# Kernel tuning notes

Measured on AMD Instinct MI355X. Metric: run time of the kernel, lower is better.

## Reference

```python
import jax, jax.numpy as jnp
import numpy as np

C = 128      # out_channels
G = 4        # RecConvLayer num_groups
BS, CIN, H, W = 4, 3, 96, 96
GN = 8
EPS = 1e-5


def _conv2d(x, w, b, pad):
    out = jax.lax.conv_general_dilated(
        x, w, (1, 1), [(pad, pad), (pad, pad)],
        dimension_numbers=("NCHW", "OIHW", "NCHW"))
    return out + b[None, :, None, None]


def _prelu(x, a):
    return jnp.maximum(x, 0) + a[0] * jnp.minimum(x, 0)


def _group_norm(x, w, b):
    bs, c, h, wd = x.shape
    xg = x.reshape(bs, GN, c // GN, h, wd)
    mu = xg.mean(axis=(2, 3, 4), keepdims=True)
    var = xg.var(axis=(2, 3, 4), keepdims=True)  # biased, as torch GroupNorm
    xn = ((xg - mu) * jax.lax.rsqrt(var + EPS)).reshape(bs, c, h, wd)
    return xn * w[None, :, None, None] + b[None, :, None, None]


def _single_conv(x, w, b, a, gw, gb, pad):
    # SingleConvLayer in eval mode: Conv2d -> PReLU -> GroupNorm (no noise)
    return _group_norm(_prelu(_conv2d(x, w, b, pad), a), gw, gb)


def _bidir_gru_layer(x, wih, whh, bih, bhh):
    # x: (T,B,Din); wih: (2,3C,Din); whh: (2,3C,C); bih/bhh: (2,3C)
    Cc = whh.shape[-1]
    h0 = jnp.zeros((x.shape[1], Cc), x.dtype)

    def run_dir(gx, wh, bh):
        def step(h, g):
            gh = h @ wh.T + bh
            r = jax.nn.sigmoid(g[:, :Cc] + gh[:, :Cc])
            z = jax.nn.sigmoid(g[:, Cc:2 * Cc] + gh[:, Cc:2 * Cc])
            n = jnp.tanh(g[:, 2 * Cc:] + r * gh[:, 2 * Cc:])
            hn = (1.0 - z) * n + z * h
            return hn, hn
        return jax.lax.scan(step, h0, gx)[1]

    yf = run_dir(x @ wih[0].T + bih[0], whh[0], bhh[0])
    yb = run_dir(x[::-1] @ wih[1].T + bih[1], whh[1], bhh[1])[::-1]
    return jnp.concatenate([yf, yb], axis=-1)  # (T,B,2C)


def _gru2(x, wih0, whh0, bih0, bhh0, wih1, whh1, bih1, bhh1):
    y = _bidir_gru_layer(x, wih0, whh0, bih0, bhh0)
    return _bidir_gru_layer(y, wih1, whh1, bih1, bhh1)


_gru_groups = jax.vmap(_gru2, in_axes=(1, 0, 0, 0, 0, 0, 0, 0, 0), out_axes=1)


def _run_gru(x_tgbc, p):
    out = _gru_groups(x_tgbc, *p)               # (T,G,B,2C)
    t, g, b, _ = out.shape
    return out.reshape(t, g, b, 2, -1).mean(axis=3)  # mean over directions -> (T,G,B,C)


def _forward(x, conv1_w, conv1_b, prelu1_a, gn1_w, gn1_b,
             conv2_w, conv2_b, prelu2_a, gn2_w, gn2_b,
             comb_w, comb_b, prelu3_a, gn3_w, gn3_b,
             h_wih0, h_whh0, h_bih0, h_bhh0, h_wih1, h_whh1, h_bih1, h_bhh1,
             v_wih0, v_whh0, v_bih0, v_bhh0, v_wih1, v_whh1, v_bih1, v_bhh1,
             h1_wih0, h1_whh0, h1_bih0, h1_bhh0, h1_wih1, h1_whh1, h1_bih1, h1_bhh1,
             v1_wih0, v1_whh0, v1_bih0, v1_bhh0, v1_wih1, v1_whh1, v1_bih1, v1_bhh1):
    x = _single_conv(x, conv1_w, conv1_b, prelu1_a, gn1_w, gn1_b, 1)
    x = _single_conv(x, conv2_w, conv2_b, prelu2_a, gn2_w, gn2_b, 1)
    bs, c, m, n = x.shape
    vg, hg = n // G, m // G
    y = jnp.transpose(x, (0, 3, 2, 1))                               # (bs,n,m,c)
    y1 = jnp.transpose(y.reshape(bs, G, vg * m, c), (2, 1, 0, 3))    # vertical seqs (m*vg,G,bs,c)
    ym = jnp.transpose(y, (0, 2, 1, 3))                              # (bs,m,n,c)
    y2 = jnp.transpose(ym.reshape(bs, G, hg * n, c), (2, 1, 0, 3))   # horizontal seqs (n*hg,G,bs,c)

    hn = _run_gru(y2, (h_wih0, h_whh0, h_bih0, h_bhh0, h_wih1, h_whh1, h_bih1, h_bhh1))
    vn = _run_gru(y1, (v_wih0, v_whh0, v_bih0, v_bhh0, v_wih1, v_whh1, v_bih1, v_bhh1))

    hn_b = jnp.transpose(hn, (2, 1, 0, 3)).reshape(bs, m, n, c)
    y1b = jnp.transpose(jnp.transpose(hn_b, (0, 2, 1, 3)).reshape(bs, G, vg * m, c), (2, 1, 0, 3))
    vn_b = jnp.transpose(vn, (2, 1, 0, 3)).reshape(bs, n, m, c)
    y2b = jnp.transpose(jnp.transpose(vn_b, (0, 2, 1, 3)).reshape(bs, G, hg * n, c), (2, 1, 0, 3))

    hn2 = _run_gru(y2b, (h1_wih0, h1_whh0, h1_bih0, h1_bhh0, h1_wih1, h1_whh1, h1_bih1, h1_bhh1))
    vn2 = _run_gru(y1b, (v1_wih0, v1_whh0, v1_bih0, v1_bhh0, v1_wih1, v1_whh1, v1_bih1, v1_bhh1))

    hcnm = jnp.transpose(jnp.transpose(hn2, (2, 1, 0, 3)).reshape(bs, m, n, c), (0, 3, 1, 2))  # (bs,c,m,n)
    vcnm = jnp.transpose(jnp.transpose(vn2, (2, 1, 0, 3)).reshape(bs, n, m, c), (0, 3, 2, 1))  # (bs,c,m,n)
    return _single_conv(jnp.concatenate([hcnm, vcnm], axis=1), comb_w, comb_b, prelu3_a, gn3_w, gn3_b, 0)


def setup_inputs() -> dict:
    key = jax.random.key(0)
    ks = jax.random.split(key, 8)
    nrm = lambda k, s, sc: jax.random.normal(k, s, jnp.float32) * sc
    inp = {
        "x": nrm(ks[0], (BS, CIN, H, W), 1.0),
        "conv1_w": nrm(ks[1], (C, CIN, 3, 3), 0.1), "conv1_b": nrm(ks[2], (C,), 0.05),
        "prelu1_a": jnp.full((1,), 0.25, jnp.float32),
        "gn1_w": jnp.ones((C,), jnp.float32), "gn1_b": jnp.zeros((C,), jnp.float32),
        "conv2_w": nrm(ks[3], (C, C, 3, 3), 0.03), "conv2_b": nrm(ks[4], (C,), 0.05),
        "prelu2_a": jnp.full((1,), 0.25, jnp.float32),
        "gn2_w": jnp.ones((C,), jnp.float32), "gn2_b": jnp.zeros((C,), jnp.float32),
        "comb_w": nrm(ks[5], (C, 2 * C, 1, 1), 0.05), "comb_b": nrm(ks[6], (C,), 0.05),
        "prelu3_a": jnp.full((1,), 0.25, jnp.float32),
        "gn3_w": jnp.ones((C,), jnp.float32), "gn3_b": jnp.zeros((C,), jnp.float32),
    }
    shapes = [("wih0", (G, 2, 3 * C, C)), ("whh0", (G, 2, 3 * C, C)),
              ("bih0", (G, 2, 3 * C)), ("bhh0", (G, 2, 3 * C)),
              ("wih1", (G, 2, 3 * C, 2 * C)), ("whh1", (G, 2, 3 * C, C)),
              ("bih1", (G, 2, 3 * C)), ("bhh1", (G, 2, 3 * C))]
    for i, p in enumerate(["h", "v", "h1", "v1"]):
        kp = jax.random.split(jax.random.fold_in(key, 100 + i), 8)
        for j, (nm, sh) in enumerate(shapes):
            inp[p + "_" + nm] = nrm(kp[j], sh, 0.05)
    return inp


def reference(x, conv1_w, conv1_b, prelu1_a, gn1_w, gn1_b,
              conv2_w, conv2_b, prelu2_a, gn2_w, gn2_b,
              comb_w, comb_b, prelu3_a, gn3_w, gn3_b,
              h_wih0, h_whh0, h_bih0, h_bhh0, h_wih1, h_whh1, h_bih1, h_bhh1,
              v_wih0, v_whh0, v_bih0, v_bhh0, v_wih1, v_whh1, v_bih1, v_bhh1,
              h1_wih0, h1_whh0, h1_bih0, h1_bhh0, h1_wih1, h1_whh1, h1_bih1, h1_bhh1,
              v1_wih0, v1_whh0, v1_bih0, v1_bhh0, v1_wih1, v1_whh1, v1_bih1, v1_bhh1):
    return _forward(x, conv1_w, conv1_b, prelu1_a, gn1_w, gn1_b,
                    conv2_w, conv2_b, prelu2_a, gn2_w, gn2_b,
                    comb_w, comb_b, prelu3_a, gn3_w, gn3_b,
                    h_wih0, h_whh0, h_bih0, h_bhh0, h_wih1, h_whh1, h_bih1, h_bhh1,
                    v_wih0, v_whh0, v_bih0, v_bhh0, v_wih1, v_whh1, v_bih1, v_bhh1,
                    h1_wih0, h1_whh0, h1_bih0, h1_bhh0, h1_wih1, h1_whh1, h1_bih1, h1_bhh1,
                    v1_wih0, v1_whh0, v1_bih0, v1_bhh0, v1_wih1, v1_whh1, v1_bih1, v1_bhh1)
```

## Files before the change

kernel.cpp:

```cpp
#include <hip/hip_runtime.h>

typedef unsigned short u16;
typedef __attribute__((ext_vector_type(8))) short bf16x8;
typedef __attribute__((ext_vector_type(4))) float f32x4;
typedef __attribute__((ext_vector_type(4))) int   i32x4;

#define DEVFN static __device__ __forceinline__
#define AS_G __attribute__((address_space(1)))
#define AS_L __attribute__((address_space(3)))

DEVFN float b2f(u16 u){ return __uint_as_float(((unsigned int)u)<<16); }
DEVFN u16 f2b(float f){ unsigned int x = __float_as_uint(f); x += 0x7FFFu + ((x>>16)&1u); return (u16)(x>>16); }
DEVFN float fastrcp(float x){ return __builtin_amdgcn_rcpf(x); }

struct CastArgs { const float* s[8]; u16* d[8]; int n[8]; };
__global__ void castf2b_g(CastArgs a)
{
    int p = blockIdx.y;
    int i = blockIdx.x*256 + threadIdx.x;
    if (i < a.n[p]) a.d[p][i] = f2b(a.s[p][i]);
}

struct QuantArgs { const float* w[8]; char* q[8]; float* dq[8]; };
__global__ void quant_whh_g(QuantArgs a)
{
    int p = blockIdx.y;
    int row = blockIdx.x;
    int lane = threadIdx.x;
    const float* wr = a.w[p] + (long long)row*128;
    float v0 = wr[lane], v1 = wr[lane+64];
    float m = fmaxf(fabsf(v0), fabsf(v1));
#pragma unroll
    for (int off = 32; off; off >>= 1) m = fmaxf(m, __shfl_xor(m, off));
    float s = (m > 0.f) ? m * (1.f/127.f) : 1.f;
    float inv = 1.f / s;
    a.q[p][(long long)row*128 + lane]      = (char)__float2int_rn(v0 * inv);
    a.q[p][(long long)row*128 + lane + 64] = (char)__float2int_rn(v1 * inv);
    if (lane == 0) a.dq[p][row] = s * (1.f/127.f);
}

__global__ __launch_bounds__(256)
void gemm_bt(const u16* __restrict__ A, const u16* __restrict__ B,
             const float* __restrict__ bias, u16* __restrict__ C,
             int K, int N,
             long long zA, long long zB, long long zBias, long long zC,
             const float* __restrict__ alphaP, float* __restrict__ stats, int rowsPerB,
             const u16* __restrict__ Ax, const u16* __restrict__ Bx,
             const float* __restrict__ biasx, u16* __restrict__ Cx, int zHalf)
{
    __shared__ __align__(16) u16 As[128*32];
    __shared__ __align__(16) u16 Bs[128*32];
    __shared__ float sstat[16];

    const int tid  = threadIdx.x;
    const int wave = tid >> 6, lane = tid & 63;
    const int quad = lane >> 4, l16 = lane & 15;
    const int wm = wave & 1, wn = wave >> 1;

    long long z = blockIdx.z;
    const u16* Ap = A; const u16* Bp = B; const float* bp = bias; u16* Cp = C;
    if (Ax && z >= zHalf) { Ap = Ax; Bp = Bx; bp = biasx; Cp = Cx; z -= zHalf; }
    Ap += z * zA; Bp += z * zB; Cp += z * zC;
    if (bp) bp += z * zBias;

    const int lin   = blockIdx.y * gridDim.x + blockIdx.x;
    const int mBase = (int)(lin / gridDim.y) * 128;
    const int nBase = (int)(lin % gridDim.y) * 128;

    f32x4 acc[4][4];
#pragma unroll
    for (int i = 0; i < 4; i++)
#pragma unroll
        for (int j = 0; j < 4; j++) acc[i][j] = (f32x4){0.f,0.f,0.f,0.f};

    const int srow = lane >> 2;
    const int sk   = (lane & 3) * 8;
    const int nK = K >> 5;

    for (int kk = 0; kk < nK; ++kk) {
        const int k0 = kk << 5;
#pragma unroll
        for (int q = 0; q < 2; q++) {
            const u16* ga = Ap + (long long)(mBase + wave*32 + q*16 + srow) * K + k0 + sk;
            const u16* gb = Bp + (long long)(nBase + wave*32 + q*16 + srow) * K + k0 + sk;
            __builtin_amdgcn_global_load_lds((const AS_G unsigned int*)ga,
                (AS_L unsigned int*)(As + (wave*32 + q*16)*32), 16, 0, 0);
            __builtin_amdgcn_global_load_lds((const AS_G unsigned int*)gb,
                (AS_L unsigned int*)(Bs + (wave*32 + q*16)*32), 16, 0, 0);
        }
        __syncthreads();
        bf16x8 af[4], bfr[4];
#pragma unroll
        for (int mt = 0; mt < 4; mt++) af[mt]  = *(const bf16x8*)(As + (wm*64 + mt*16 + l16)*32 + quad*8);
#pragma unroll
        for (int nt = 0; nt < 4; nt++) bfr[nt] = *(const bf16x8*)(Bs + (wn*64 + nt*16 + l16)*32 + quad*8);
#pragma unroll
        for (int mt = 0; mt < 4; mt++)
#pragma unroll
            for (int nt = 0; nt < 4; nt++)
                acc[mt][nt] = __builtin_amdgcn_mfma_f32_16x16x32_bf16(bfr[nt], af[mt], acc[mt][nt], 0, 0, 0);
        __syncthreads();
    }

    const bool doStats = (stats != nullptr);
    const float alpha = alphaP ? alphaP[0] : 0.f;
    if (doStats) { if (tid < 16) sstat[tid] = 0.f; __syncthreads(); }

    float lsum[4] = {0,0,0,0}, lsq[4] = {0,0,0,0};
#pragma unroll
    for (int nt = 0; nt < 4; nt++) {
        const int col0 = nBase + wn*64 + nt*16 + quad*4;
        float4 bv4 = {0.f, 0.f, 0.f, 0.f};
        if (bp) bv4 = *(const float4*)(bp + col0);
#pragma unroll
        for (int mt = 0; mt < 4; mt++) {
            const int row = mBase + wm*64 + mt*16 + l16;
            float v0 = acc[mt][nt][0] + bv4.x;
            float v1 = acc[mt][nt][1] + bv4.y;
            float v2 = acc[mt][nt][2] + bv4.z;
            float v3 = acc[mt][nt][3] + bv4.w;
            if (alphaP) {
                v0 = v0 > 0.f ? v0 : alpha * v0;
                v1 = v1 > 0.f ? v1 : alpha * v1;
                v2 = v2 > 0.f ? v2 : alpha * v2;
                v3 = v3 > 0.f ? v3 : alpha * v3;
            }
            if (doStats) {
                lsum[nt] += v0 + v1 + v2 + v3;
                lsq[nt]  += v0*v0 + v1*v1 + v2*v2 + v3*v3;
            }
            uint2 pk;
            pk.x = (unsigned)f2b(v0) | ((unsigned)f2b(v1) << 16);
            pk.y = (unsigned)f2b(v2) | ((unsigned)f2b(v3) << 16);
            *(uint2*)(Cp + (long long)row * N + col0) = pk;
        }
    }
    if (doStats) {
#pragma unroll
        for (int nt = 0; nt < 4; nt++) {
            const int gn = wn*4 + nt;
            atomicAdd(&sstat[gn], lsum[nt]);
            atomicAdd(&sstat[8 + gn], lsq[nt]);
        }
        __syncthreads();
        if (tid < 16) {
            const int b = mBase / rowsPerB;
            atomicAdd(&stats[b*16 + tid], sstat[tid]);
        }
    }
}

#define HSB 144
#define BURST 16
#define NCHUNK 16
#define CHUNK  144
#define WARM   112

__global__ __launch_bounds__(512, 2)
void gru_rec(const u16* __restrict__ gxH, const u16* __restrict__ gxV,
             const char* __restrict__ qwH, const char* __restrict__ qwV,
             const float* __restrict__ dqH, const float* __restrict__ dqV,
             const float* __restrict__ bhhH, const float* __restrict__ bhhV,
             u16* __restrict__ outH, u16* __restrict__ outV)
{
    const int id    = blockIdx.x / NCHUNK;
    const int chunk = blockIdx.x % NCHUNK;
    const int stack = id >> 3, g = (id >> 1) & 3, d = id & 1;
    const u16*  gx  = (stack ? gxV : gxH) + (long long)g*9216*768 + d*384;
    const char* qw  = (stack ? qwV : qwH) + (long long)(g*2 + d)*384*128;
    const float* dqv = (stack ? dqV : dqH) + (g*2 + d)*384;
    const float* bhh = (stack ? bhhV : bhhH) + (g*2 + d)*384;
    u16* out = (stack ? outV : outH) + (long long)g*9216*256 + d*128;

    const int sBegin = chunk * CHUNK;
    const int sEnd   = sBegin + CHUNK;
    const int sw     = (chunk == 0) ? 0 : sBegin - WARM;

    const int tid = threadIdx.x;
    const int w = tid >> 6, lane = tid & 63;
    const int quad = lane >> 4, l16 = lane & 15;

    __shared__ __align__(16) char hbf8[2][16*HSB];
    __shared__ __align__(16) u16 outs[2][BURST*512];
    for (int i = tid; i < 2*16*HSB; i += 512) ((char*)hbf8)[i] = 0;

    const int col = w*16 + l16;
    i32x4 ifrag[3][2];
#pragma unroll
    for (int gate = 0; gate < 3; ++gate)
#pragma unroll
        for (int kc = 0; kc < 2; ++kc)
            ifrag[gate][kc] = *(const i32x4*)(qw + (long long)(gate*128 + col)*128 + kc*64 + quad*16);

    const float dqR = dqv[col], dqZ = dqv[128 + col], dqN = dqv[256 + col];
    const float bhr = bhh[col], bhz = bhh[128 + col], bhn = bhh[256 + col];
    float h = 0.f;

    const int step = d ? -1 : 1;
    const int t0 = d ? 2303 : 0;
    const long long rowStride = (long long)step * 3072;

    u16 bankA[BURST][3], bankB[BURST][3];
    const i32x4 zi = {0,0,0,0};

    auto loadBank = [&](u16 (&bk)[BURST][3], int sbase) {
        if (sbase >= sEnd) return;
        const u16* p = gx + (long long)((t0 + step*sbase)*4 + quad)*768 + col;
#pragma unroll
        for (int j = 0; j < BURST; j++) {
            bk[j][0] = p[0]; bk[j][1] = p[128]; bk[j][2] = p[256];
            p += rowStride;
        }
    };

    auto flushOut = [&](int sbase, int bank) {
        const u16* ob = outs[bank];
#pragma unroll
        for (int c = 0; c < 2; c++) {
            const int lin = (tid + c*512) * 8;
            const int s   = lin >> 9;
            const int rem = lin & 511;
            const int q   = rem >> 7, cc = rem & 127;
            const int tt  = t0 + step * (sbase + s);
            *(uint4*)(out + (long long)(tt*4 + q)*256 + cc) = *(const uint4*)(ob + lin);
        }
    };

    auto ldsbar = [&]() {
        asm volatile("s_waitcnt lgkmcnt(0)\n\ts_barrier" ::: "memory");
    };

    auto stepf = [&](int j, int bank, u16 g0, u16 g1, u16 g2) {
        const char* hb = hbf8[j & 1];
        char* hw = (char*)hbf8[(j + 1) & 1];
        i32x4 a0 = *(const i32x4*)(hb + l16*HSB + quad*16);
        i32x4 a1 = *(const i32x4*)(hb + l16*HSB + 64 + quad*16);
        i32x4 aR = __builtin_amdgcn_mfma_i32_16x16x64_i8(a0, ifrag[0][0], zi, 0, 0, 0);
        i32x4 aZ = __builtin_amdgcn_mfma_i32_16x16x64_i8(a0, ifrag[1][0], zi, 0, 0, 0);
        i32x4 aN = __builtin_amdgcn_mfma_i32_16x16x64_i8(a0, ifrag[2][0], zi, 0, 0, 0);
        aR = __builtin_amdgcn_mfma_i32_16x16x64_i8(a1, ifrag[0][1], aR, 0, 0, 0);
        aZ = __builtin_amdgcn_mfma_i32_16x16x64_i8(a1, ifrag[1][1], aZ, 0, 0, 0);
        aN = __builtin_amdgcn_mfma_i32_16x16x64_i8(a1, ifrag[2][1], aN, 0, 0, 0);
        float r  = fastrcp(1.f + __expf(-(b2f(g0) + bhr + (float)aR[0] * dqR)));
        float zz = fastrcp(1.f + __expf(-(b2f(g1) + bhz + (float)aZ[0] * dqZ)));
        float nn = b2f(g2) + r * ((float)aN[0] * dqN + bhn);
        nn = 1.f - 2.f * fastrcp(__expf(2.f * nn) + 1.f);
        h = zz * (h - nn) + nn;
        hw[4*quad*HSB + col] = (char)__float2int_rn(h * 127.f);
        outs[bank][j*512 + quad*128 + col] = f2b(h);
        ldsbar();
    };

    loadBank(bankA, sw);
    __syncthreads();

    for (int base = sw; base < sEnd; base += 2*BURST) {
        loadBank(bankB, base + BURST);
#pragma unroll
        for (int j = 0; j < BURST; j++) stepf(j, 0, bankA[j][0], bankA[j][1], bankA[j][2]);
        if (base >= sBegin) flushOut(base, 0);
        loadBank(bankA, base + 2*BURST);
#pragma unroll
        for (int j = 0; j < BURST; j++) stepf(j, 1, bankB[j][0], bankB[j][1], bankB[j][2]);
        const int b2s = base + BURST;
        if (b2s >= sBegin && b2s < sEnd) flushOut(b2s, 1);
    }
}

__global__ void repack_w(const float* __restrict__ w1, const float* __restrict__ w2,
                         const float* __restrict__ wc,
                         u16* __restrict__ w1r, u16* __restrict__ w2r, u16* __restrict__ wcr)
{
    int idx = blockIdx.x*256 + threadIdx.x;
    if (idx < 128*1152) {
        int o = idx / 1152, k = idx % 1152, tap = k >> 7, ci = k & 127;
        w2r[idx] = f2b(w2[(o*128 + ci)*9 + tap]);
    }
    if (idx < 128*32) {
        int o = idx >> 5, k = idx & 31;
        float v = 0.f;
        if (k < 27) { int tap = k/3, ci = k - tap*3; v = w1[(o*3 + ci)*9 + tap]; }
        w1r[idx] = f2b(v);
    }
    if (idx < 128*256) wcr[idx] = f2b(wc[idx]);
}

__global__ void im2col1(const float* __restrict__ x, u16* __restrict__ A1)
{
    int row = blockIdx.x*256 + threadIdx.x;
    if (row >= 36864) return;
    int b = row / 9216, rem = row % 9216, m = rem / 96, n = rem % 96;
    u16* dst = A1 + (long long)row*32;
#pragma unroll
    for (int k = 0; k < 32; k++) {
        float v = 0.f;
        if (k < 27) {
            int tap = k/3, ci = k - tap*3;
            int mm = m + tap/3 - 1, nn = n + tap%3 - 1;
            if (mm >= 0 && mm < 96 && nn >= 0 && nn < 96)
                v = x[((b*3 + ci)*96 + mm)*96 + nn];
        }
        dst[k] = f2b(v);
    }
}

__global__ void make_ss(const float* __restrict__ stats, const float* __restrict__ gw,
                        const float* __restrict__ gb, float* __restrict__ sc,
                        float* __restrict__ sh, float invCnt)
{
    int idx = blockIdx.x*256 + threadIdx.x;
    if (idx >= 512) return;
    int b = idx >> 7, c = idx & 127, gn = c >> 4;
    float s = stats[b*16 + gn], q = stats[b*16 + 8 + gn];
    float mu = s * invCnt, var = fmaxf(q * invCnt - mu*mu, 0.f);
    float rstd = rsqrtf(var + 1e-5f);
    float scale = rstd * gw[c];
    sc[idx] = scale;
    sh[idx] = gb[c] - mu * scale;
}

__global__ void im2col2(const u16* __restrict__ buf1, const float* __restrict__ sc,
                        const float* __restrict__ sh, u16* __restrict__ A2)
{
    int idx = blockIdx.x*256 + threadIdx.x;
    int row = idx / 144, q = idx % 144;
    int tap = q >> 4, ci0 = (q & 15) << 3;
    int b = row / 9216, rem = row % 9216, m = rem / 96, n = rem % 96;
    int mm = m + tap/3 - 1, nn = n + tap%3 - 1;
    bf16x8 o = (bf16x8){0,0,0,0,0,0,0,0};
    if (mm >= 0 && mm < 96 && nn >= 0 && nn < 96) {
        bf16x8 v = *(const bf16x8*)(buf1 + (long long)(b*9216 + mm*96 + nn)*128 + ci0);
#pragma unroll
        for (int j = 0; j < 8; j++)
            o[j] = (short)f2b(b2f((u16)v[j]) * sc[b*128 + ci0 + j] + sh[b*128 + ci0 + j]);
    }
    *(bf16x8*)(A2 + (long long)row*1152 + tap*128 + ci0) = o;
}

__global__ void repack_seq(const u16* __restrict__ buf2, const float* __restrict__ sc,
                           const float* __restrict__ sh, u16* __restrict__ xh, u16* __restrict__ xv)
{
    int idx = blockIdx.x*256 + threadIdx.x;
    int c0 = (idx & 15) << 3, r1 = idx >> 4;
    int b = r1 & 3, r2 = r1 >> 2;
    int t = r2 % 2304, g = r2 / 2304;
    int iw = t / 96, pos = t % 96;
    int rowH = b*9216 + (g*24 + iw)*96 + pos;
    int rowV = b*9216 + pos*96 + (g*24 + iw);
    bf16x8 vh = *(const bf16x8*)(buf2 + (long long)rowH*128 + c0);
    bf16x8 vv = *(const bf16x8*)(buf2 + (long long)rowV*128 + c0);
    bf16x8 oh, ov;
#pragma unroll
    for (int j = 0; j < 8; j++) {
        float scale = sc[b*128 + c0 + j], shift = sh[b*128 + c0 + j];
        oh[j] = (short)f2b(b2f((u16)vh[j]) * scale + shift);
        ov[j] = (short)f2b(b2f((u16)vv[j]) * scale + shift);
    }
    *(bf16x8*)(xh + ((long long)r1 << 7) + c0) = oh;
    *(bf16x8*)(xv + ((long long)r1 << 7) + c0) = ov;
}

__global__ void repack_B(const u16* __restrict__ z1H, const u16* __restrict__ z1V,
                         u16* __restrict__ xh2, u16* __restrict__ xv2)
{
    int idx = blockIdx.x*256 + threadIdx.x;
    int c0 = (idx & 15) << 3, r1 = idx >> 4;
    int b = r1 & 3, r2 = r1 >> 2;
    int t = r2 % 2304, g = r2 / 2304;
    {
        int ih2 = t / 96, n = t % 96, gs = n / 24, iv = n % 24;
        long long s = ((long long)gs*9216 + (iv*96 + g*24 + ih2)*4 + b)*256 + c0;
        bf16x8 a = *(const bf16x8*)(z1V + s);
        bf16x8 bb = *(const bf16x8*)(z1V + s + 128);
        bf16x8 o;
#pragma unroll
        for (int j = 0; j < 8; j++) o[j] = (short)f2b(0.5f*(b2f((u16)a[j]) + b2f((u16)bb[j])));
        *(bf16x8*)(xh2 + ((long long)r1 << 7) + c0) = o;
    }
    {
        int iv = t / 96, m = t % 96, gs = m / 24, ih = m % 24;
        long long s = ((long long)gs*9216 + (ih*96 + g*24 + iv)*4 + b)*256 + c0;
        bf16x8 a = *(const bf16x8*)(z1H + s);
        bf16x8 bb = *(const bf16x8*)(z1H + s + 128);
        bf16x8 o;
#pragma unroll
        for (int j = 0; j < 8; j++) o[j] = (short)f2b(0.5f*(b2f((u16)a[j]) + b2f((u16)bb[j])));
        *(bf16x8*)(xv2 + ((long long)r1 << 7) + c0) = o;
    }
}

__global__ void repack_comb(const u16* __restrict__ z1H, const u16* __restrict__ z1V,
                            u16* __restrict__ Ac)
{
    int idx = blockIdx.x*256 + threadIdx.x;
    int k0 = (idx & 31) << 3;
    int row = idx >> 5;
    int b = row / 9216, rem = row % 9216, m = rem / 96, n = rem % 96;
    const u16* src;
    long long s;
    if (k0 < 128) {
        int g = m / 24, ih = m % 24, ts = ih*96 + n;
        s = ((long long)g*9216 + ts*4 + b)*256 + k0;
        src = z1H;
    } else {
        int c = k0 - 128, g = n / 24, iv = n % 24, ts = iv*96 + m;
        s = ((long long)g*9216 + ts*4 + b)*256 + c;
        src = z1V;
    }
    bf16x8 a = *(const bf16x8*)(src + s);
    bf16x8 bb = *(const bf16x8*)(src + s + 128);
    bf16x8 o;
#pragma unroll
    for (int j = 0; j < 8; j++) o[j] = (short)f2b(0.5f*(b2f((u16)a[j]) + b2f((u16)bb[j])));
    *(bf16x8*)(Ac + (long long)row*256 + k0) = o;
}

__global__ void final_kernel(const u16* __restrict__ p3, const float* __restrict__ sc,
                             const float* __restrict__ sh, float* __restrict__ out)
{
    __shared__ float tile[128*97];
    int bm = blockIdx.x;
    int b = bm / 96, m = bm % 96;
    int tid = threadIdx.x;
    int rowbase = b*9216 + m*96;
    for (int idx = tid; idx < 96*128; idx += 256) {
        int n = idx >> 7, o = idx & 127;
        float v = b2f(p3[(long long)(rowbase + n)*128 + o]);
        tile[o*97 + n] = v * sc[b*128 + o] + sh[b*128 + o];
    }
    __syncthreads();
    for (int idx = tid; idx < 96*128; idx += 256) {
        int o = idx / 96, n = idx % 96;
        out[((long long)(b*128 + o)*96 + m)*96 + n] = tile[o*97 + n];
    }
}

extern "C" void kernel_launch(void* const* d_in, const int* in_sizes, int n_in,
                              void* d_out, int out_size, void* d_ws, size_t ws_size,
                              hipStream_t stream)
{
    (void)in_sizes; (void)n_in; (void)out_size;
    auto F = [&](int i){ return (const float*)d_in[i]; };

    char* ws = (char*)d_ws;
    size_t off = 0;
    auto alloc = [&](size_t bytes)->char* {
        char* p = ws + off;
        off += (bytes + 255) & ~(size_t)255;
        return p;
    };

    float* stats = (float*)alloc(3*64*sizeof(float));
    float* sc1 = (float*)alloc(512*4); float* sh1 = (float*)alloc(512*4);
    float* sc2 = (float*)alloc(512*4); float* sh2 = (float*)alloc(512*4);
    float* sc3 = (float*)alloc(512*4); float* sh3 = (float*)alloc(512*4);
    u16* w1r  = (u16*)alloc((size_t)128*32*2);
    u16* w2r  = (u16*)alloc((size_t)128*1152*2);
    u16* wcr  = (u16*)alloc((size_t)128*256*2);
    u16 *wih0c[4], *wih1c[4];
    char *qw0[4], *qw1[4];
    float *dq0[4], *dq1[4];
    for (int p = 0; p < 4; p++) {
        wih0c[p] = (u16*)alloc((size_t)393216*2);
        wih1c[p] = (u16*)alloc((size_t)786432*2);
        qw0[p]   = (char*)alloc((size_t)393216);
        qw1[p]   = (char*)alloc((size_t)393216);
        dq0[p]   = (float*)alloc((size_t)3072*4);
        dq1[p]   = (float*)alloc((size_t)3072*4);
    }
    u16* A1   = (u16*)alloc((size_t)36864*32*2);
    u16* buf1 = (u16*)alloc((size_t)36864*128*2);
    u16* buf2 = (u16*)alloc((size_t)36864*128*2);
    u16* xh   = (u16*)alloc((size_t)4718592*2);
    u16* xv   = (u16*)alloc((size_t)4718592*2);
    u16* gxH  = (u16*)alloc((size_t)4*9216*768*2);
    u16* gxV  = (u16*)alloc((size_t)4*9216*768*2);
    u16* z1H  = (u16*)alloc((size_t)4*9216*256*2);
    u16* z1V  = (u16*)alloc((size_t)4*9216*256*2);

    u16* A2  = gxH;
    u16* y0H = xh;
    u16* y0V = buf1;
    u16* Ac  = xh;
    u16* p3  = buf1;

    if (ws_size < off) return;

    hipMemsetAsync(stats, 0, 3*64*sizeof(float), stream);
    repack_w<<<576, 256, 0, stream>>>(F(1), F(6), F(11), w1r, w2r, wcr);
    im2col1<<<144, 256, 0, stream>>>(F(0), A1);

    CastArgs ca;
    QuantArgs qa;
    for (int p = 0; p < 4; p++) {
        int base = 16 + p*8;
        ca.s[p]   = F(base+0); ca.d[p]   = wih0c[p]; ca.n[p]   = 393216;
        ca.s[p+4] = F(base+4); ca.d[p+4] = wih1c[p]; ca.n[p+4] = 786432;
        qa.w[p]   = F(base+1); qa.q[p]   = qw0[p];   qa.dq[p]   = dq0[p];
        qa.w[p+4] = F(base+5); qa.q[p+4] = qw1[p];   qa.dq[p+4] = dq1[p];
    }
    castf2b_g<<<dim3(3072, 8), 256, 0, stream>>>(ca);
    quant_whh_g<<<dim3(3072, 8), 64, 0, stream>>>(qa);

    gemm_bt<<<dim3(288,1,1), 256, 0, stream>>>(A1, w1r, F(2), buf1, 32, 128,
        0,0,0,0, F(3), stats + 0, 9216, nullptr, nullptr, nullptr, nullptr, 0);
    make_ss<<<2, 256, 0, stream>>>(stats + 0, F(4), F(5), sc1, sh1, 1.f/147456.f);

    im2col2<<<20736, 256, 0, stream>>>(buf1, sc1, sh1, A2);
    gemm_bt<<<dim3(288,1,1), 256, 0, stream>>>(A2, w2r, F(7), buf2, 1152, 128,
        0,0,0,0, F(8), stats + 64, 9216, nullptr, nullptr, nullptr, nullptr, 0);
    make_ss<<<2, 256, 0, stream>>>(stats + 64, F(9), F(10), sc2, sh2, 1.f/147456.f);

    repack_seq<<<2304, 256, 0, stream>>>(buf2, sc2, sh2, xh, xv);

    const long long zA0 = 9216LL*128, zA1 = 9216LL*256;
    const long long zB0 = 768LL*128,  zB1 = 768LL*256;
    const long long zC  = 9216LL*768;

    gemm_bt<<<dim3(72,6,8), 256, 0, stream>>>(xh, wih0c[0], F(18), gxH, 128, 768, zA0, zB0, 768, zC,
        nullptr, nullptr, 0, xv, wih0c[1], F(26), gxV, 4);
    gru_rec<<<16*NCHUNK, 512, 0, stream>>>(gxH, gxV, qw0[0], qw0[1], dq0[0], dq0[1], F(19), F(27), y0H, y0V);
    gemm_bt<<<dim3(72,6,8), 256, 0, stream>>>(y0H, wih1c[0], F(22), gxH, 256, 768, zA1, zB1, 768, zC,
        nullptr, nullptr, 0, y0V, wih1c[1], F(30), gxV, 4);
    gru_rec<<<16*NCHUNK, 512, 0, stream>>>(gxH, gxV, qw1[0], qw1[1], dq1[0], dq1[1], F(23), F(31), z1H, z1V);

    repack_B<<<2304, 256, 0, stream>>>(z1H, z1V, xh, xv);
    gemm_bt<<<dim3(72,6,8), 256, 0, stream>>>(xh, wih0c[2], F(34), gxH, 128, 768, zA0, zB0, 768, zC,
        nullptr, nullptr, 0, xv, wih0c[3], F(42), gxV, 4);
    gru_rec<<<16*NCHUNK, 512, 0, stream>>>(gxH, gxV, qw0[2], qw0[3], dq0[2], dq0[3], F(35), F(43), y0H, y0V);
    gemm_bt<<<dim3(72,6,8), 256, 0, stream>>>(y0H, wih1c[2], F(38), gxH, 256, 768, zA1, zB1, 768, zC,
        nullptr, nullptr, 0, y0V, wih1c[3], F(46), gxV, 4);
    gru_rec<<<16*NCHUNK, 512, 0, stream>>>(gxH, gxV, qw1[2], qw1[3], dq1[2], dq1[3], F(39), F(47), z1H, z1V);

    repack_comb<<<4608, 256, 0, stream>>>(z1H, z1V, Ac);
    gemm_bt<<<dim3(288,1,1), 256, 0, stream>>>(Ac, wcr, F(12), p3, 256, 128,
        0,0,0,0, F(13), stats + 128, 9216, nullptr, nullptr, nullptr, nullptr, 0);
    make_ss<<<2, 256, 0, stream>>>(stats + 128, F(14), F(15), sc3, sh3, 1.f/147456.f);
    final_kernel<<<384, 256, 0, stream>>>(p3, sc3, sh3, (float*)d_out);
}
```

Measured before the change: 961.4 us.

## Fuse direction-mean repacks into GEMM A-loads via gathered addressing and duplicated weights

Removes the repack_B and repack_comb kernels. The GEMMs now read the bidirectional GRU outputs directly through gathered row addresses (gmode 1 and 2). The mean over directions is folded into the weights by duplicating each input-weight column scaled by 0.5, which doubles K from 128 to 256 and from 256 to 512. This saves the intermediate write and re-read of the averaged tensors and two launches, at the cost of more MFMA work and less contiguous A-side loads in those GEMMs.

```diff
diff --git a/kernel.cpp b/kernel.cpp
--- a/kernel.cpp
+++ b/kernel.cpp
@@ -13,12 +13,18 @@
 DEVFN u16 f2b(float f){ unsigned int x = __float_as_uint(f); x += 0x7FFFu + ((x>>16)&1u); return (u16)(x>>16); }
 DEVFN float fastrcp(float x){ return __builtin_amdgcn_rcpf(x); }
 
-struct CastArgs { const float* s[8]; u16* d[8]; int n[8]; };
+struct CastArgs { const float* s[8]; u16* d[8]; int n[8]; int dup[8]; };
 __global__ void castf2b_g(CastArgs a)
 {
     int p = blockIdx.y;
     int i = blockIdx.x*256 + threadIdx.x;
-    if (i < a.n[p]) a.d[p][i] = f2b(a.s[p][i]);
+    if (i >= a.n[p]) return;
+    if (a.dup[p]) {
+        int src = ((i >> 8) << 7) + (i & 127);
+        a.d[p][i] = f2b(0.5f * a.s[p][src]);
+    } else {
+        a.d[p][i] = f2b(a.s[p][i]);
+    }
 }
 
 struct QuantArgs { const float* w[8]; char* q[8]; float* dq[8]; };
@@ -46,7 +52,8 @@
              long long zA, long long zB, long long zBias, long long zC,
              const float* __restrict__ alphaP, float* __restrict__ stats, int rowsPerB,
              const u16* __restrict__ Ax, const u16* __restrict__ Bx,
-             const float* __restrict__ biasx, u16* __restrict__ Cx, int zHalf)
+             const float* __restrict__ biasx, u16* __restrict__ Cx, int zHalf,
+             int gmode, const u16* __restrict__ gSrc1, const u16* __restrict__ gSrc2)
 {
     __shared__ __align__(16) u16 As[128*32];
     __shared__ __align__(16) u16 Bs[128*32];
@@ -58,8 +65,9 @@
     const int wm = wave & 1, wn = wave >> 1;
 
     long long z = blockIdx.z;
+    bool second = false;
     const u16* Ap = A; const u16* Bp = B; const float* bp = bias; u16* Cp = C;
-    if (Ax && z >= zHalf) { Ap = Ax; Bp = Bx; bp = biasx; Cp = Cx; z -= zHalf; }
+    if (Ax && z >= zHalf) { second = true; Ap = Ax; Bp = Bx; bp = biasx; Cp = Cx; z -= zHalf; }
     Ap += z * zA; Bp += z * zB; Cp += z * zC;
     if (bp) bp += z * zBias;
 
@@ -67,25 +75,55 @@
     const int mBase = (int)(lin / gridDim.y) * 128;
     const int nBase = (int)(lin % gridDim.y) * 128;
 
-    f32x4 acc[4][4];
-#pragma unroll
-    for (int i = 0; i < 4; i++)
-#pragma unroll
-        for (int j = 0; j < 4; j++) acc[i][j] = (f32x4){0.f,0.f,0.f,0.f};
-
     const int srow = lane >> 2;
     const int sk   = (lane & 3) * 8;
     const int nK = K >> 5;
 
+    const u16* gb[2];
+    const u16* gb2[2];
+    if (gmode) {
+#pragma unroll
+        for (int q = 0; q < 2; q++) {
+            const int row = mBase + wave*32 + q*16 + srow;
+            if (gmode == 1) {
+                const int b = row & 3, t = row >> 2;
+                long long s0;
+                if (!second) { int ih2 = t/96, n = t%96, gs = n/24, iv = n%24;
+                               s0 = (long long)gs*9216 + (long long)(iv*96 + (int)z*24 + ih2)*4 + b; }
+                else         { int iv = t/96, m = t%96, gs = m/24, ih = m%24;
+                               s0 = (long long)gs*9216 + (long long)(ih*96 + (int)z*24 + iv)*4 + b; }
+                gb[q] = (second ? gSrc2 : gSrc1) + s0*256;
+            } else {
+                const int b = row/9216, rem = row%9216, m = rem/96, n = rem%96;
+                int gH = m/24, ih = m%24;
+                long long sH = (long long)gH*9216 + (long long)(ih*96 + n)*4 + b;
+                int gV = n/24, iv = n%24;
+                long long sV = (long long)gV*9216 + (long long)(iv*96 + m)*4 + b;
+                gb[q]  = gSrc1 + sH*256;
+                gb2[q] = gSrc2 + sV*256 - 256;
+            }
+        }
+    }
+
+    f32x4 acc[4][4];
+#pragma unroll
+    for (int i = 0; i < 4; i++)
+#pragma unroll
+        for (int j = 0; j < 4; j++) acc[i][j] = (f32x4){0.f,0.f,0.f,0.f};
+
     for (int kk = 0; kk < nK; ++kk) {
         const int k0 = kk << 5;
 #pragma unroll
         for (int q = 0; q < 2; q++) {
-            const u16* ga = Ap + (long long)(mBase + wave*32 + q*16 + srow) * K + k0 + sk;
-            const u16* gb = Bp + (long long)(nBase + wave*32 + q*16 + srow) * K + k0 + sk;
+            const u16* ga;
+            if (gmode == 0)
+                ga = Ap + (long long)(mBase + wave*32 + q*16 + srow) * K + k0 + sk;
+            else
+                ga = ((gmode == 2 && k0 >= 256) ? gb2[q] : gb[q]) + k0 + sk;
+            const u16* gbB = Bp + (long long)(nBase + wave*32 + q*16 + srow) * K + k0 + sk;
             __builtin_amdgcn_global_load_lds((const AS_G unsigned int*)ga,
                 (AS_L unsigned int*)(As + (wave*32 + q*16)*32), 16, 0, 0);
-            __builtin_amdgcn_global_load_lds((const AS_G unsigned int*)gb,
+            __builtin_amdgcn_global_load_lds((const AS_G unsigned int*)gbB,
                 (AS_L unsigned int*)(Bs + (wave*32 + q*16)*32), 16, 0, 0);
         }
         __syncthreads();
@@ -282,7 +320,11 @@
         if (k < 27) { int tap = k/3, ci = k - tap*3; v = w1[(o*3 + ci)*9 + tap]; }
         w1r[idx] = f2b(v);
     }
-    if (idx < 128*256) wcr[idx] = f2b(wc[idx]);
+    if (idx < 128*512) {
+        int o = idx >> 9, k = idx & 511;
+        int c = ((k >> 8) << 7) + (k & 127);
+        wcr[idx] = f2b(0.5f * wc[o*256 + c]);
+    }
 }
 
 __global__ void im2col1(const float* __restrict__ x, u16* __restrict__ A1)
@@ -360,61 +402,6 @@
     *(bf16x8*)(xv + ((long long)r1 << 7) + c0) = ov;
 }
 
-__global__ void repack_B(const u16* __restrict__ z1H, const u16* __restrict__ z1V,
-                         u16* __restrict__ xh2, u16* __restrict__ xv2)
-{
-    int idx = blockIdx.x*256 + threadIdx.x;
-    int c0 = (idx & 15) << 3, r1 = idx >> 4;
-    int b = r1 & 3, r2 = r1 >> 2;
-    int t = r2 % 2304, g = r2 / 2304;
-    {
-        int ih2 = t / 96, n = t % 96, gs = n / 24, iv = n % 24;
-        long long s = ((long long)gs*9216 + (iv*96 + g*24 + ih2)*4 + b)*256 + c0;
-        bf16x8 a = *(const bf16x8*)(z1V + s);
-        bf16x8 bb = *(const bf16x8*)(z1V + s + 128);
-        bf16x8 o;
-#pragma unroll
-        for (int j = 0; j < 8; j++) o[j] = (short)f2b(0.5f*(b2f((u16)a[j]) + b2f((u16)bb[j])));
-        *(bf16x8*)(xh2 + ((long long)r1 << 7) + c0) = o;
-    }
-    {
-        int iv = t / 96, m = t % 96, gs = m / 24, ih = m % 24;
-        long long s = ((long long)gs*9216 + (ih*96 + g*24 + iv)*4 + b)*256 + c0;
-        bf16x8 a = *(const bf16x8*)(z1H + s);
-        bf16x8 bb = *(const bf16x8*)(z1H + s + 128);
-        bf16x8 o;
-#pragma unroll
-        for (int j = 0; j < 8; j++) o[j] = (short)f2b(0.5f*(b2f((u16)a[j]) + b2f((u16)bb[j])));
-        *(bf16x8*)(xv2 + ((long long)r1 << 7) + c0) = o;
-    }
-}
-
-__global__ void repack_comb(const u16* __restrict__ z1H, const u16* __restrict__ z1V,
-                            u16* __restrict__ Ac)
-{
-    int idx = blockIdx.x*256 + threadIdx.x;
-    int k0 = (idx & 31) << 3;
-    int row = idx >> 5;
-    int b = row / 9216, rem = row % 9216, m = rem / 96, n = rem % 96;
-    const u16* src;
-    long long s;
-    if (k0 < 128) {
-        int g = m / 24, ih = m % 24, ts = ih*96 + n;
-        s = ((long long)g*9216 + ts*4 + b)*256 + k0;
-        src = z1H;
-    } else {
-        int c = k0 - 128, g = n / 24, iv = n % 24, ts = iv*96 + m;
-        s = ((long long)g*9216 + ts*4 + b)*256 + c;
-        src = z1V;
-    }
-    bf16x8 a = *(const bf16x8*)(src + s);
-    bf16x8 bb = *(const bf16x8*)(src + s + 128);
-    bf16x8 o;
-#pragma unroll
-    for (int j = 0; j < 8; j++) o[j] = (short)f2b(0.5f*(b2f((u16)a[j]) + b2f((u16)bb[j])));
-    *(bf16x8*)(Ac + (long long)row*256 + k0) = o;
-}
-
 __global__ void final_kernel(const u16* __restrict__ p3, const float* __restrict__ sc,
                              const float* __restrict__ sh, float* __restrict__ out)
 {
@@ -456,12 +443,12 @@
     float* sc3 = (float*)alloc(512*4); float* sh3 = (float*)alloc(512*4);
     u16* w1r  = (u16*)alloc((size_t)128*32*2);
     u16* w2r  = (u16*)alloc((size_t)128*1152*2);
-    u16* wcr  = (u16*)alloc((size_t)128*256*2);
+    u16* wcr  = (u16*)alloc((size_t)128*512*2);
     u16 *wih0c[4], *wih1c[4];
     char *qw0[4], *qw1[4];
     float *dq0[4], *dq1[4];
     for (int p = 0; p < 4; p++) {
-        wih0c[p] = (u16*)alloc((size_t)393216*2);
+        wih0c[p] = (u16*)alloc((size_t)(p < 2 ? 393216 : 786432)*2);
         wih1c[p] = (u16*)alloc((size_t)786432*2);
         qw0[p]   = (char*)alloc((size_t)393216);
         qw1[p]   = (char*)alloc((size_t)393216);
@@ -481,7 +468,6 @@
     u16* A2  = gxH;
     u16* y0H = xh;
     u16* y0V = buf1;
-    u16* Ac  = xh;
     u16* p3  = buf1;
 
     if (ws_size < off) return;
@@ -494,8 +480,10 @@
     QuantArgs qa;
     for (int p = 0; p < 4; p++) {
         int base = 16 + p*8;
-        ca.s[p]   = F(base+0); ca.d[p]   = wih0c[p]; ca.n[p]   = 393216;
-        ca.s[p+4] = F(base+4); ca.d[p+4] = wih1c[p]; ca.n[p+4] = 786432;
+        ca.s[p]   = F(base+0); ca.d[p]   = wih0c[p];
+        ca.n[p]   = (p < 2) ? 393216 : 786432;
+        ca.dup[p] = (p < 2) ? 0 : 1;
+        ca.s[p+4] = F(base+4); ca.d[p+4] = wih1c[p]; ca.n[p+4] = 786432; ca.dup[p+4] = 0;
         qa.w[p]   = F(base+1); qa.q[p]   = qw0[p];   qa.dq[p]   = dq0[p];
         qa.w[p+4] = F(base+5); qa.q[p+4] = qw1[p];   qa.dq[p+4] = dq1[p];
     }
@@ -503,12 +491,14 @@
     quant_whh_g<<<dim3(3072, 8), 64, 0, stream>>>(qa);
 
     gemm_bt<<<dim3(288,1,1), 256, 0, stream>>>(A1, w1r, F(2), buf1, 32, 128,
-        0,0,0,0, F(3), stats + 0, 9216, nullptr, nullptr, nullptr, nullptr, 0);
+        0,0,0,0, F(3), stats + 0, 9216, nullptr, nullptr, nullptr, nullptr, 0,
+        0, nullptr, nullptr);
     make_ss<<<2, 256, 0, stream>>>(stats + 0, F(4), F(5), sc1, sh1, 1.f/147456.f);
 
     im2col2<<<20736, 256, 0, stream>>>(buf1, sc1, sh1, A2);
     gemm_bt<<<dim3(288,1,1), 256, 0, stream>>>(A2, w2r, F(7), buf2, 1152, 128,
-        0,0,0,0, F(8), stats + 64, 9216, nullptr, nullptr, nullptr, nullptr, 0);
+        0,0,0,0, F(8), stats + 64, 9216, nullptr, nullptr, nullptr, nullptr, 0,
+        0, nullptr, nullptr);
     make_ss<<<2, 256, 0, stream>>>(stats + 64, F(9), F(10), sc2, sh2, 1.f/147456.f);
 
     repack_seq<<<2304, 256, 0, stream>>>(buf2, sc2, sh2, xh, xv);
@@ -518,23 +508,22 @@
     const long long zC  = 9216LL*768;
 
     gemm_bt<<<dim3(72,6,8), 256, 0, stream>>>(xh, wih0c[0], F(18), gxH, 128, 768, zA0, zB0, 768, zC,
-        nullptr, nullptr, 0, xv, wih0c[1], F(26), gxV, 4);
+        nullptr, nullptr, 0, xv, wih0c[1], F(26), gxV, 4, 0, nullptr, nullptr);
     gru_rec<<<16*NCHUNK, 512, 0, stream>>>(gxH, gxV, qw0[0], qw0[1], dq0[0], dq0[1], F(19), F(27), y0H, y0V);
     gemm_bt<<<dim3(72,6,8), 256, 0, stream>>>(y0H, wih1c[0], F(22), gxH, 256, 768, zA1, zB1, 768, zC,
-        nullptr, nullptr, 0, y0V, wih1c[1], F(30), gxV, 4);
+        nullptr, nullptr, 0, y0V, wih1c[1], F(30), gxV, 4, 0, nullptr, nullptr);
     gru_rec<<<16*NCHUNK, 512, 0, stream>>>(gxH, gxV, qw1[0], qw1[1], dq1[0], dq1[1], F(23), F(31), z1H, z1V);
 
-    repack_B<<<2304, 256, 0, stream>>>(z1H, z1V, xh, xv);
-    gemm_bt<<<dim3(72,6,8), 256, 0, stream>>>(xh, wih0c[2], F(34), gxH, 128, 768, zA0, zB0, 768, zC,
-        nullptr, nullptr, 0, xv, wih0c[3], F(42), gxV, 4);
+    gemm_bt<<<dim3(72,6,8), 256, 0, stream>>>(z1H, wih0c[2], F(34), gxH, 256, 768, 0, 768LL*256, 768, zC,
+        nullptr, nullptr, 0, z1H, wih0c[3], F(42), gxV, 4, 1, z1V, z1H);
     gru_rec<<<16*NCHUNK, 512, 0, stream>>>(gxH, gxV, qw0[2], qw0[3], dq0[2], dq0[3], F(35), F(43), y0H, y0V);
     gemm_bt<<<dim3(72,6,8), 256, 0, stream>>>(y0H, wih1c[2], F(38), gxH, 256, 768, zA1, zB1, 768, zC,
-        nullptr, nullptr, 0, y0V, wih1c[3], F(46), gxV, 4);
+        nullptr, nullptr, 0, y0V, wih1c[3], F(46), gxV, 4, 0, nullptr, nullptr);
     gru_rec<<<16*NCHUNK, 512, 0, stream>>>(gxH, gxV, qw1[2], qw1[3], dq1[2], dq1[3], F(39), F(47), z1H, z1V);
 
-    repack_comb<<<4608, 256, 0, stream>>>(z1H, z1V, Ac);
-    gemm_bt<<<dim3(288,1,1), 256, 0, stream>>>(Ac, wcr, F(12), p3, 256, 128,
-        0,0,0,0, F(13), stats + 128, 9216, nullptr, nullptr, nullptr, nullptr, 0);
+    gemm_bt<<<dim3(288,1,1), 256, 0, stream>>>(z1H, wcr, F(12), p3, 512, 128,
+        0,0,0,0, F(13), stats + 128, 9216, nullptr, nullptr, nullptr, nullptr, 0,
+        2, z1H, z1V);
     make_ss<<<2, 256, 0, stream>>>(stats + 128, F(14), F(15), sc3, sh3, 1.f/147456.f);
     final_kernel<<<384, 256, 0, stream>>>(p3, sc3, sh3, (float*)d_out);
 }
```

Result: no change. 964.0 us (+0.3%).
